# Optimization experiments

Hardware: AMD Instinct MI355X
Metric: run time of the kernel (lower is better)

## Reference

```python
import jax, jax.numpy as jnp
import numpy as np

N_NODES = 50000
N_EDGES = 1600000
N_FEAT, N_HID, N_CLASS = 256, 128, 64


def setup_inputs() -> dict:
    key = jax.random.key(0)
    ks = jax.random.split(key, 8)
    x = jax.random.normal(ks[0], (N_NODES, N_FEAT), dtype=jnp.float32)
    edge_index = jax.random.randint(ks[1], (2, N_EDGES), 0, N_NODES, dtype=jnp.int64)
    edge_weight = jax.random.uniform(ks[2], (N_EDGES,), dtype=jnp.float32)
    # Glorot-style init for GCNConv weights, zero bias (PyG defaults)
    W1 = jax.random.normal(ks[3], (N_FEAT, N_HID), dtype=jnp.float32) * (1.0 / np.sqrt(N_FEAT))
    b1 = jnp.zeros((N_HID,), dtype=jnp.float32)
    W2 = jax.random.normal(ks[4], (N_HID, N_CLASS), dtype=jnp.float32) * (1.0 / np.sqrt(N_HID))
    b2 = jnp.zeros((N_CLASS,), dtype=jnp.float32)
    return {"x": x, "edge_index": edge_index, "edge_weight": edge_weight,
            "W1": W1, "b1": b1, "W2": W2, "b2": b2}


def _gcn_norm(edge_index, edge_weight, num_nodes):
    # add self loops with weight 1 (GCNConv add_self_loops=True)
    loop = jnp.arange(num_nodes, dtype=edge_index.dtype)
    row = jnp.concatenate([edge_index[0], loop])
    col = jnp.concatenate([edge_index[1], loop])
    ew = jnp.concatenate([edge_weight, jnp.ones((num_nodes,), dtype=edge_weight.dtype)])
    # symmetric normalization: deg computed on target (col) nodes
    deg = jax.ops.segment_sum(ew, col, num_segments=num_nodes)
    dinv = jnp.where(deg > 0, jax.lax.rsqrt(deg), 0.0)
    norm = dinv[row] * ew * dinv[col]
    return row, col, norm


def _gcn_conv(h, row, col, norm, W, b, num_nodes):
    h = h @ W                       # [N, out]
    msgs = h[row] * norm[:, None]   # [E+N, out] gather + scale
    out = jax.ops.segment_sum(msgs, col, num_segments=num_nodes)  # scatter-add to targets
    return out + b


def reference(x, edge_index, edge_weight, W1, b1, W2, b2):
    n = x.shape[0]
    row, col, norm = _gcn_norm(edge_index, edge_weight, n)
    h = jax.nn.sigmoid(_gcn_conv(x, row, col, norm, W1, b1, n))
    out = jnp.tanh(_gcn_conv(h, row, col, norm, W2, b2, n))
    return out
```

## Files before the change

kernel.cpp:

```cpp
#include <hip/hip_runtime.h>
#include <math.h>

#define N_NODES 50000
#define N_EDGES 1600000
#define N_FEAT  256
#define N_HID   128
#define N_CLASS 64
#define SCAN_NBLK ((N_NODES + 1023) / 1024)
#define FIXSCALE 268435456.0f

__device__ __forceinline__ unsigned short f2bf(float f) {
  unsigned int u = __float_as_uint(f);
  unsigned int r = (u + 0x7fffu + ((u >> 16) & 1u)) >> 16;
  return (unsigned short)r;
}

__global__ __launch_bounds__(256) void deg_rank_kernel(
    const int* __restrict__ col, const float* __restrict__ ew,
    unsigned long long* __restrict__ packed, unsigned short* __restrict__ rank, int E) {
  int e = blockIdx.x * 256 + threadIdx.x;
  if (e >= E) return;
  int c = col[e];
  unsigned long long fix = (unsigned long long)__float2uint_rn(ew[e] * FIXSCALE);
  unsigned long long old = atomicAdd(&packed[c], (1ULL << 40) | fix);
  rank[e] = (unsigned short)(old >> 40);
}

__global__ __launch_bounds__(256) void scan1_kernel(
    const unsigned long long* __restrict__ packed, int* __restrict__ rowptr,
    int* __restrict__ partials, float* __restrict__ dinv) {
  __shared__ int wsum[4];
  __shared__ int woff[4];
  int t = threadIdx.x, b = blockIdx.x;
  int base = b * 1024 + t * 4;
  int v0 = 0, v1 = 0, v2 = 0, v3 = 0;
#pragma unroll
  for (int j = 0; j < 4; ++j) {
    int i = base + j;
    if (i < N_NODES) {
      unsigned long long p = packed[i];
      int c = (int)(p >> 40);
      float deg = (float)(long long)(p & 0xFFFFFFFFFFULL) * (1.0f / FIXSCALE);
      dinv[i] = rsqrtf(deg + 1.0f);
      if (j == 0) v0 = c; else if (j == 1) v1 = c; else if (j == 2) v2 = c; else v3 = c;
    }
  }
  int s1 = v0 + v1, s2 = s1 + v2, s3 = s2 + v3;
  int lane = t & 63, w = t >> 6;
  int inc = s3;
#pragma unroll
  for (int off = 1; off < 64; off <<= 1) {
    int u = __shfl_up(inc, off, 64);
    if (lane >= off) inc += u;
  }
  if (lane == 63) wsum[w] = inc;
  __syncthreads();
  if (t == 0) {
    int a = 0;
#pragma unroll
    for (int i = 0; i < 4; ++i) { woff[i] = a; a += wsum[i]; }
    partials[b] = a;
  }
  __syncthreads();
  int ex = woff[w] + inc - s3;
  if (base + 0 < N_NODES) rowptr[base + 0] = ex;
  if (base + 1 < N_NODES) rowptr[base + 1] = ex + v0;
  if (base + 2 < N_NODES) rowptr[base + 2] = ex + s1;
  if (base + 3 < N_NODES) rowptr[base + 3] = ex + s2;
}

__global__ void scan2_kernel(int* __restrict__ partials, int* __restrict__ rowptr) {
  if (threadIdx.x == 0 && blockIdx.x == 0) {
    int a = 0;
    for (int i = 0; i < SCAN_NBLK; ++i) { int x = partials[i]; partials[i] = a; a += x; }
    rowptr[N_NODES] = a;
  }
}

__global__ __launch_bounds__(256) void scan3_kernel(
    int* __restrict__ rowptr, const int* __restrict__ partials) {
  int i = blockIdx.x * 256 + threadIdx.x;
  if (i < N_NODES) rowptr[i] += partials[i >> 10];
}

__global__ __launch_bounds__(256) void scatter_kernel(
    const int* __restrict__ row, const int* __restrict__ col,
    const float* __restrict__ ew, const unsigned short* __restrict__ rank,
    const float* __restrict__ dinv, const int* __restrict__ rowptr,
    int2* __restrict__ ep, int E) {
  int e = blockIdx.x * 256 + threadIdx.x;
  if (e >= E) return;
  int r = row[e], c = col[e];
  float w = dinv[r] * ew[e] * dinv[c];
  int pos = rowptr[c] + (int)rank[e];
  ep[pos] = make_int2(r, __float_as_int(w));
}

template <int BN, int BK, int K>
__global__ __launch_bounds__(256) void gemm_kernel(
    const float* __restrict__ A, const float* __restrict__ B,
    unsigned short* __restrict__ C, int M) {
  constexpr int BM = 64;
  constexpr int TC = BN / 4;
  constexpr int TR = 256 / TC;
  constexpr int RM = BM / TR;
  __shared__ float As[BM][BK + 4];
  __shared__ float Bs[BK][BN];

  int t  = threadIdx.x;
  int m0 = blockIdx.x * BM;
  int tc = t % TC, tr = t / TC;

  float acc[RM][4];
#pragma unroll
  for (int r = 0; r < RM; ++r)
#pragma unroll
    for (int c = 0; c < 4; ++c) acc[r][c] = 0.f;

  for (int k0 = 0; k0 < K; k0 += BK) {
    constexpr int F4R = BK / 4;
#pragma unroll
    for (int p = 0; p < (BM * F4R) / 256; ++p) {
      int row = t / F4R + p * (256 / F4R);
      int c4  = t % F4R;
      int gr  = m0 + row;
      float4 v = make_float4(0.f, 0.f, 0.f, 0.f);
      if (gr < M) v = *(const float4*)&A[(size_t)gr * K + k0 + c4 * 4];
      *(float4*)&As[row][c4 * 4] = v;
    }
    constexpr int BF4 = BK * BN / 4;
#pragma unroll
    for (int p = 0; p < BF4 / 256; ++p) {
      int idx = p * 256 + t;
      int row = idx / (BN / 4), c4 = idx % (BN / 4);
      *(float4*)&Bs[row][c4 * 4] = *(const float4*)&B[(size_t)(k0 + row) * BN + c4 * 4];
    }
    __syncthreads();

    for (int kk = 0; kk < BK; kk += 4) {
      float4 b0 = *(const float4*)&Bs[kk + 0][tc * 4];
      float4 b1 = *(const float4*)&Bs[kk + 1][tc * 4];
      float4 b2 = *(const float4*)&Bs[kk + 2][tc * 4];
      float4 b3 = *(const float4*)&Bs[kk + 3][tc * 4];
#pragma unroll
      for (int r = 0; r < RM; ++r) {
        float4 a = *(const float4*)&As[tr * RM + r][kk];
        acc[r][0] = fmaf(a.x, b0.x, fmaf(a.y, b1.x, fmaf(a.z, b2.x, fmaf(a.w, b3.x, acc[r][0]))));
        acc[r][1] = fmaf(a.x, b0.y, fmaf(a.y, b1.y, fmaf(a.z, b2.y, fmaf(a.w, b3.y, acc[r][1]))));
        acc[r][2] = fmaf(a.x, b0.z, fmaf(a.y, b1.z, fmaf(a.z, b2.z, fmaf(a.w, b3.z, acc[r][2]))));
        acc[r][3] = fmaf(a.x, b0.w, fmaf(a.y, b1.w, fmaf(a.z, b2.w, fmaf(a.w, b3.w, acc[r][3]))));
      }
    }
    __syncthreads();
  }
#pragma unroll
  for (int r = 0; r < RM; ++r) {
    int gr = m0 + tr * RM + r;
    if (gr < M) {
      uint2 o;
      o.x = (unsigned int)f2bf(acc[r][0]) | ((unsigned int)f2bf(acc[r][1]) << 16);
      o.y = (unsigned int)f2bf(acc[r][2]) | ((unsigned int)f2bf(acc[r][3]) << 16);
      *(uint2*)&C[(size_t)gr * BN + tc * 4] = o;
    }
  }
}

__global__ __launch_bounds__(256) void agg128_kernel(
    const unsigned short* __restrict__ h, const int* __restrict__ rowptr,
    const int2* __restrict__ ep, const float* __restrict__ dinv,
    const float* __restrict__ bias, float* __restrict__ out, int n) {
  int wid  = (int)((blockIdx.x * 256 + threadIdx.x) >> 6);
  int lane = threadIdx.x & 63;
  if (wid >= n) return;
  int s = rowptr[wid], e_end = rowptr[wid + 1];
  unsigned int f2 = 2u * lane;
  float a0 = 0.f, a1 = 0.f, b0 = 0.f, b1 = 0.f,
        c0 = 0.f, c1 = 0.f, d0 = 0.f, d1 = 0.f;
  int e = s;
  for (; e + 3 < e_end; e += 4) {
    int2 p0 = ep[e], p1 = ep[e + 1], p2 = ep[e + 2], p3 = ep[e + 3];
    unsigned int h0 = *(const unsigned int*)(h + ((size_t)p0.x << 7) + f2);
    unsigned int h1 = *(const unsigned int*)(h + ((size_t)p1.x << 7) + f2);
    unsigned int h2 = *(const unsigned int*)(h + ((size_t)p2.x << 7) + f2);
    unsigned int h3 = *(const unsigned int*)(h + ((size_t)p3.x << 7) + f2);
    float w0 = __int_as_float(p0.y), w1 = __int_as_float(p1.y);
    float w2 = __int_as_float(p2.y), w3 = __int_as_float(p3.y);
    a0 = fmaf(w0, __uint_as_float(h0 << 16), a0);
    a1 = fmaf(w0, __uint_as_float(h0 & 0xffff0000u), a1);
    b0 = fmaf(w1, __uint_as_float(h1 << 16), b0);
    b1 = fmaf(w1, __uint_as_float(h1 & 0xffff0000u), b1);
    c0 = fmaf(w2, __uint_as_float(h2 << 16), c0);
    c1 = fmaf(w2, __uint_as_float(h2 & 0xffff0000u), c1);
    d0 = fmaf(w3, __uint_as_float(h3 << 16), d0);
    d1 = fmaf(w3, __uint_as_float(h3 & 0xffff0000u), d1);
  }
  for (; e < e_end; ++e) {
    int2 p0 = ep[e];
    unsigned int h0 = *(const unsigned int*)(h + ((size_t)p0.x << 7) + f2);
    float w0 = __int_as_float(p0.y);
    a0 = fmaf(w0, __uint_as_float(h0 << 16), a0);
    a1 = fmaf(w0, __uint_as_float(h0 & 0xffff0000u), a1);
  }
  float di = dinv[wid], sw = di * di;
  unsigned int hs = *(const unsigned int*)(h + ((size_t)wid << 7) + f2);
  a0 = fmaf(sw, __uint_as_float(hs << 16), a0);
  a1 = fmaf(sw, __uint_as_float(hs & 0xffff0000u), a1);
  float v0 = (a0 + b0) + (c0 + d0) + bias[f2];
  float v1 = (a1 + b1) + (c1 + d1) + bias[f2 + 1];
  v0 = 1.f / (1.f + expf(-v0));
  v1 = 1.f / (1.f + expf(-v1));
  *(float2*)&out[((size_t)wid << 7) + f2] = make_float2(v0, v1);
}

__global__ __launch_bounds__(256) void agg64_kernel(
    const unsigned short* __restrict__ h, const int* __restrict__ rowptr,
    const int2* __restrict__ ep, const float* __restrict__ dinv,
    const float* __restrict__ bias, float* __restrict__ out, int n) {
  int wid  = (int)((blockIdx.x * 256 + threadIdx.x) >> 6);
  int lane = threadIdx.x & 63;
  if (wid >= n) return;
  int half = lane >> 5, ll = lane & 31;
  unsigned int f2 = 2u * ll;
  int s = rowptr[wid], e_end = rowptr[wid + 1];
  float a0 = 0.f, a1 = 0.f, b0 = 0.f, b1 = 0.f,
        c0 = 0.f, c1 = 0.f, d0 = 0.f, d1 = 0.f;
  int e = s + half;
  for (; e + 6 < e_end; e += 8) {
    int2 p0 = ep[e], p1 = ep[e + 2], p2 = ep[e + 4], p3 = ep[e + 6];
    unsigned int h0 = *(const unsigned int*)(h + ((size_t)p0.x << 6) + f2);
    unsigned int h1 = *(const unsigned int*)(h + ((size_t)p1.x << 6) + f2);
    unsigned int h2 = *(const unsigned int*)(h + ((size_t)p2.x << 6) + f2);
    unsigned int h3 = *(const unsigned int*)(h + ((size_t)p3.x << 6) + f2);
    float w0 = __int_as_float(p0.y), w1 = __int_as_float(p1.y);
    float w2 = __int_as_float(p2.y), w3 = __int_as_float(p3.y);
    a0 = fmaf(w0, __uint_as_float(h0 << 16), a0);
    a1 = fmaf(w0, __uint_as_float(h0 & 0xffff0000u), a1);
    b0 = fmaf(w1, __uint_as_float(h1 << 16), b0);
    b1 = fmaf(w1, __uint_as_float(h1 & 0xffff0000u), b1);
    c0 = fmaf(w2, __uint_as_float(h2 << 16), c0);
    c1 = fmaf(w2, __uint_as_float(h2 & 0xffff0000u), c1);
    d0 = fmaf(w3, __uint_as_float(h3 << 16), d0);
    d1 = fmaf(w3, __uint_as_float(h3 & 0xffff0000u), d1);
  }
  for (; e < e_end; e += 2) {
    int2 p0 = ep[e];
    unsigned int h0 = *(const unsigned int*)(h + ((size_t)p0.x << 6) + f2);
    float w0 = __int_as_float(p0.y);
    a0 = fmaf(w0, __uint_as_float(h0 << 16), a0);
    a1 = fmaf(w0, __uint_as_float(h0 & 0xffff0000u), a1);
  }
  a0 = (a0 + b0) + (c0 + d0);
  a1 = (a1 + b1) + (c1 + d1);
  if (half == 0) {
    float di = dinv[wid], sw = di * di;
    unsigned int hs = *(const unsigned int*)(h + ((size_t)wid << 6) + f2);
    a0 = fmaf(sw, __uint_as_float(hs << 16), a0);
    a1 = fmaf(sw, __uint_as_float(hs & 0xffff0000u), a1);
  }
  a0 += __shfl_xor(a0, 32, 64);
  a1 += __shfl_xor(a1, 32, 64);
  if (half == 0) {
    float v0 = tanhf(a0 + bias[f2]);
    float v1 = tanhf(a1 + bias[f2 + 1]);
    *(float2*)&out[(size_t)wid * 64 + f2] = make_float2(v0, v1);
  }
}

extern "C" void kernel_launch(void* const* d_in, const int* in_sizes, int n_in,
                              void* d_out, int out_size, void* d_ws, size_t ws_size,
                              hipStream_t stream) {
  const float* x  = (const float*)d_in[0];
  const int*   ei = (const int*)d_in[1];
  const float* ew = (const float*)d_in[2];
  const float* W1 = (const float*)d_in[3];
  const float* b1 = (const float*)d_in[4];
  const float* W2 = (const float*)d_in[5];
  const float* b2 = (const float*)d_in[6];
  float* out = (float*)d_out;

  const int* row = ei;
  const int* col = ei + N_EDGES;

  char* ws = (char*)d_ws;
  size_t off = 0;
  auto alloc = [&](size_t bytes) {
    void* p = ws + off;
    off = (off + bytes + 255) & ~(size_t)255;
    return p;
  };
  unsigned long long* packed = (unsigned long long*)alloc(N_NODES * 8);
  int*   rowptr   = (int*)alloc((N_NODES + 1) * 4);
  float* dinv     = (float*)alloc(N_NODES * 4);
  int*   partials = (int*)alloc(SCAN_NBLK * 4);
  unsigned short* rank = (unsigned short*)alloc((size_t)N_EDGES * 2);
  int2*  ep       = (int2*)alloc((size_t)N_EDGES * 8);
  unsigned short* bufA = (unsigned short*)alloc((size_t)N_NODES * N_HID * 2);
  float*          bufB = (float*)alloc((size_t)N_NODES * N_HID * 4);
  unsigned short* bufC = (unsigned short*)alloc((size_t)N_NODES * N_CLASS * 2);

  hipMemsetAsync(packed, 0, N_NODES * 8, stream);

  int eblocks = (N_EDGES + 255) / 256;
  int nblocks = (N_NODES + 255) / 256;
  int gblocks = (N_NODES + 63) / 64;

  deg_rank_kernel<<<eblocks, 256, 0, stream>>>(col, ew, packed, rank, N_EDGES);
  scan1_kernel<<<SCAN_NBLK, 256, 0, stream>>>(packed, rowptr, partials, dinv);
  scan2_kernel<<<1, 64, 0, stream>>>(partials, rowptr);
  scan3_kernel<<<nblocks, 256, 0, stream>>>(rowptr, partials);
  scatter_kernel<<<eblocks, 256, 0, stream>>>(row, col, ew, rank, dinv, rowptr, ep, N_EDGES);

  gemm_kernel<N_HID, 64, N_FEAT><<<gblocks, 256, 0, stream>>>(x, W1, bufA, N_NODES);
  agg128_kernel<<<(N_NODES * 64 + 255) / 256, 256, 0, stream>>>(
      bufA, rowptr, ep, dinv, b1, bufB, N_NODES);

  gemm_kernel<N_CLASS, 64, N_HID><<<gblocks, 256, 0, stream>>>(bufB, W2, bufC, N_NODES);
  agg64_kernel<<<(N_NODES * 64 + 255) / 256, 256, 0, stream>>>(
      bufC, rowptr, ep, dinv, b2, out, N_NODES);
}
```

Measured before the change: 398.3 us.

## Use bf16 MFMA GEMMs with transposed bf16 weights and bf16 hidden activations

Replaces the fp32 FMA tiled GEMMs with a bf16 MFMA (16x16x32) kernel. The A and B tiles sit in swizzled LDS, and the weights are pre-transposed and converted to bf16 by a new small kernel. The first aggregation now writes its sigmoid output as bf16 instead of fp32, which halves the intermediate buffer traffic and lets the second GEMM read bf16 directly. The cost is lower precision on the inputs and the hidden layer, plus two extra tiny launches. Output stores are now scalar 16-bit writes.

Result: faster. 350.0 us (-12.1%).

```diff
diff --git a/kernel.cpp b/kernel.cpp
--- a/kernel.cpp
+++ b/kernel.cpp
@@ -9,10 +9,21 @@
 #define SCAN_NBLK ((N_NODES + 1023) / 1024)
 #define FIXSCALE 268435456.0f
 
-__device__ __forceinline__ unsigned short f2bf(float f) {
+typedef __attribute__((ext_vector_type(8))) short short8v;
+typedef __attribute__((ext_vector_type(4))) float float4v;
+
+__device__ __forceinline__ unsigned int f2bf(float f) {
   unsigned int u = __float_as_uint(f);
   unsigned int r = (u + 0x7fffu + ((u >> 16) & 1u)) >> 16;
-  return (unsigned short)r;
+  return r & 0xffffu;
+}
+
+__global__ __launch_bounds__(256) void transpose_w_kernel(
+    const float* __restrict__ W, unsigned short* __restrict__ WT, int K, int N) {
+  int i = blockIdx.x * 256 + threadIdx.x;
+  if (i >= N * K) return;
+  int n = i / K, k = i % K;
+  WT[i] = (unsigned short)f2bf(W[(size_t)k * N + n]);
 }
 
 __global__ __launch_bounds__(256) void deg_rank_kernel(
@@ -96,71 +107,91 @@
   ep[pos] = make_int2(r, __float_as_int(w));
 }
 
-template <int BN, int BK, int K>
-__global__ __launch_bounds__(256) void gemm_kernel(
-    const float* __restrict__ A, const float* __restrict__ B,
+template <int BN, int K, bool AFP32>
+__global__ __launch_bounds__(256) void mfma_gemm_kernel(
+    const void* __restrict__ Ain, const unsigned short* __restrict__ BT,
     unsigned short* __restrict__ C, int M) {
-  constexpr int BM = 64;
-  constexpr int TC = BN / 4;
-  constexpr int TR = 256 / TC;
-  constexpr int RM = BM / TR;
-  __shared__ float As[BM][BK + 4];
-  __shared__ float Bs[BK][BN];
-
-  int t  = threadIdx.x;
+  constexpr int BM = 64, BK = 64;
+  constexpr int NT = BN / 16;
+  __shared__ unsigned char AsB[BM * 128];
+  __shared__ unsigned char BsB[BN * 128];
+  int t = threadIdx.x;
+  int lane = t & 63, wv = t >> 6;
   int m0 = blockIdx.x * BM;
-  int tc = t % TC, tr = t / TC;
-
-  float acc[RM][4];
-#pragma unroll
-  for (int r = 0; r < RM; ++r)
-#pragma unroll
-    for (int c = 0; c < 4; ++c) acc[r][c] = 0.f;
+
+  float4v acc[NT];
+#pragma unroll
+  for (int i = 0; i < NT; ++i) acc[i] = (float4v){0.f, 0.f, 0.f, 0.f};
 
   for (int k0 = 0; k0 < K; k0 += BK) {
-    constexpr int F4R = BK / 4;
-#pragma unroll
-    for (int p = 0; p < (BM * F4R) / 256; ++p) {
-      int row = t / F4R + p * (256 / F4R);
-      int c4  = t % F4R;
-      int gr  = m0 + row;
-      float4 v = make_float4(0.f, 0.f, 0.f, 0.f);
-      if (gr < M) v = *(const float4*)&A[(size_t)gr * K + k0 + c4 * 4];
-      *(float4*)&As[row][c4 * 4] = v;
-    }
-    constexpr int BF4 = BK * BN / 4;
-#pragma unroll
-    for (int p = 0; p < BF4 / 256; ++p) {
-      int idx = p * 256 + t;
-      int row = idx / (BN / 4), c4 = idx % (BN / 4);
-      *(float4*)&Bs[row][c4 * 4] = *(const float4*)&B[(size_t)(k0 + row) * BN + c4 * 4];
+    {
+      int r = t >> 2, q = t & 3;
+      int gr = m0 + r;
+      unsigned int swz = (unsigned int)((r & 7) << 4);
+      uint4 o0 = make_uint4(0, 0, 0, 0), o1 = make_uint4(0, 0, 0, 0);
+      if constexpr (AFP32) {
+        const float* A = (const float*)Ain;
+        if (gr < M) {
+          const float* p = &A[(size_t)gr * K + k0 + q * 16];
+          float4 v0 = *(const float4*)(p + 0), v1 = *(const float4*)(p + 4);
+          float4 v2 = *(const float4*)(p + 8), v3 = *(const float4*)(p + 12);
+          o0.x = f2bf(v0.x) | (f2bf(v0.y) << 16); o0.y = f2bf(v0.z) | (f2bf(v0.w) << 16);
+          o0.z = f2bf(v1.x) | (f2bf(v1.y) << 16); o0.w = f2bf(v1.z) | (f2bf(v1.w) << 16);
+          o1.x = f2bf(v2.x) | (f2bf(v2.y) << 16); o1.y = f2bf(v2.z) | (f2bf(v2.w) << 16);
+          o1.z = f2bf(v3.x) | (f2bf(v3.y) << 16); o1.w = f2bf(v3.z) | (f2bf(v3.w) << 16);
+        }
+      } else {
+        const unsigned short* A = (const unsigned short*)Ain;
+        if (gr < M) {
+          const unsigned short* p = &A[(size_t)gr * K + k0 + q * 16];
+          o0 = *(const uint4*)(p);
+          o1 = *(const uint4*)(p + 8);
+        }
+      }
+      *(uint4*)(AsB + r * 128 + (((unsigned)(q * 32)) ^ swz)) = o0;
+      *(uint4*)(AsB + r * 128 + (((unsigned)(q * 32 + 16)) ^ swz)) = o1;
+    }
+    {
+      constexpr int BPT = BN / 2;
+      constexpr int TPR = 128 / BPT;
+      int br = t / TPR;
+      int bo = (t % TPR) * BPT;
+      unsigned int swz = (unsigned int)((br & 7) << 4);
+#pragma unroll
+      for (int s = 0; s < BPT / 16; ++s) {
+        uint4 v = *(const uint4*)&BT[(size_t)br * K + k0 + (bo + s * 16) / 2];
+        *(uint4*)(BsB + br * 128 + (((unsigned)(bo + s * 16)) ^ swz)) = v;
+      }
     }
     __syncthreads();
-
-    for (int kk = 0; kk < BK; kk += 4) {
-      float4 b0 = *(const float4*)&Bs[kk + 0][tc * 4];
-      float4 b1 = *(const float4*)&Bs[kk + 1][tc * 4];
-      float4 b2 = *(const float4*)&Bs[kk + 2][tc * 4];
-      float4 b3 = *(const float4*)&Bs[kk + 3][tc * 4];
-#pragma unroll
-      for (int r = 0; r < RM; ++r) {
-        float4 a = *(const float4*)&As[tr * RM + r][kk];
-        acc[r][0] = fmaf(a.x, b0.x, fmaf(a.y, b1.x, fmaf(a.z, b2.x, fmaf(a.w, b3.x, acc[r][0]))));
-        acc[r][1] = fmaf(a.x, b0.y, fmaf(a.y, b1.y, fmaf(a.z, b2.y, fmaf(a.w, b3.y, acc[r][1]))));
-        acc[r][2] = fmaf(a.x, b0.z, fmaf(a.y, b1.z, fmaf(a.z, b2.z, fmaf(a.w, b3.z, acc[r][2]))));
-        acc[r][3] = fmaf(a.x, b0.w, fmaf(a.y, b1.w, fmaf(a.z, b2.w, fmaf(a.w, b3.w, acc[r][3]))));
+    {
+      int ar = wv * 16 + (lane & 15);
+      int g = lane >> 4;
+      unsigned int aswz = (unsigned int)((ar & 7) << 4);
+      unsigned int bswz = (unsigned int)((lane & 7) << 4);
+#pragma unroll
+      for (int kk = 0; kk < BK; kk += 32) {
+        short8v af = *(const short8v*)(AsB + ar * 128 +
+                                       (((unsigned)(kk * 2 + g * 16)) ^ aswz));
+#pragma unroll
+        for (int nt = 0; nt < NT; ++nt) {
+          int brr = nt * 16 + (lane & 15);
+          short8v bf = *(const short8v*)(BsB + brr * 128 +
+                                         (((unsigned)(kk * 2 + g * 16)) ^ bswz));
+          acc[nt] = __builtin_amdgcn_mfma_f32_16x16x32_bf16(af, bf, acc[nt], 0, 0, 0);
+        }
       }
     }
     __syncthreads();
   }
-#pragma unroll
-  for (int r = 0; r < RM; ++r) {
-    int gr = m0 + tr * RM + r;
-    if (gr < M) {
-      uint2 o;
-      o.x = (unsigned int)f2bf(acc[r][0]) | ((unsigned int)f2bf(acc[r][1]) << 16);
-      o.y = (unsigned int)f2bf(acc[r][2]) | ((unsigned int)f2bf(acc[r][3]) << 16);
-      *(uint2*)&C[(size_t)gr * BN + tc * 4] = o;
+  int r0 = m0 + wv * 16 + (lane >> 4) * 4;
+  int c0 = lane & 15;
+#pragma unroll
+  for (int nt = 0; nt < NT; ++nt) {
+#pragma unroll
+    for (int j = 0; j < 4; ++j) {
+      int gr = r0 + j;
+      if (gr < M) C[(size_t)gr * BN + nt * 16 + c0] = (unsigned short)f2bf(acc[nt][j]);
     }
   }
 }
@@ -168,7 +199,7 @@
 __global__ __launch_bounds__(256) void agg128_kernel(
     const unsigned short* __restrict__ h, const int* __restrict__ rowptr,
     const int2* __restrict__ ep, const float* __restrict__ dinv,
-    const float* __restrict__ bias, float* __restrict__ out, int n) {
+    const float* __restrict__ bias, unsigned short* __restrict__ out, int n) {
   int wid  = (int)((blockIdx.x * 256 + threadIdx.x) >> 6);
   int lane = threadIdx.x & 63;
   if (wid >= n) return;
@@ -209,7 +240,8 @@
   float v1 = (a1 + b1) + (c1 + d1) + bias[f2 + 1];
   v0 = 1.f / (1.f + expf(-v0));
   v1 = 1.f / (1.f + expf(-v1));
-  *(float2*)&out[((size_t)wid << 7) + f2] = make_float2(v0, v1);
+  unsigned int o = f2bf(v0) | (f2bf(v1) << 16);
+  *(unsigned int*)(out + ((size_t)wid << 7) + f2) = o;
 }
 
 __global__ __launch_bounds__(256) void agg64_kernel(
@@ -294,8 +326,10 @@
   int*   partials = (int*)alloc(SCAN_NBLK * 4);
   unsigned short* rank = (unsigned short*)alloc((size_t)N_EDGES * 2);
   int2*  ep       = (int2*)alloc((size_t)N_EDGES * 8);
+  unsigned short* W1T  = (unsigned short*)alloc((size_t)N_HID * N_FEAT * 2);
+  unsigned short* W2T  = (unsigned short*)alloc((size_t)N_CLASS * N_HID * 2);
   unsigned short* bufA = (unsigned short*)alloc((size_t)N_NODES * N_HID * 2);
-  float*          bufB = (float*)alloc((size_t)N_NODES * N_HID * 4);
+  unsigned short* bufB = (unsigned short*)alloc((size_t)N_NODES * N_HID * 2);
   unsigned short* bufC = (unsigned short*)alloc((size_t)N_NODES * N_CLASS * 2);
 
   hipMemsetAsync(packed, 0, N_NODES * 8, stream);
@@ -303,6 +337,9 @@
   int eblocks = (N_EDGES + 255) / 256;
   int nblocks = (N_NODES + 255) / 256;
   int gblocks = (N_NODES + 63) / 64;
+
+  transpose_w_kernel<<<(N_HID * N_FEAT + 255) / 256, 256, 0, stream>>>(W1, W1T, N_FEAT, N_HID);
+  transpose_w_kernel<<<(N_CLASS * N_HID + 255) / 256, 256, 0, stream>>>(W2, W2T, N_HID, N_CLASS);
 
   deg_rank_kernel<<<eblocks, 256, 0, stream>>>(col, ew, packed, rank, N_EDGES);
   scan1_kernel<<<SCAN_NBLK, 256, 0, stream>>>(packed, rowptr, partials, dinv);
@@ -310,11 +347,11 @@
   scan3_kernel<<<nblocks, 256, 0, stream>>>(rowptr, partials);
   scatter_kernel<<<eblocks, 256, 0, stream>>>(row, col, ew, rank, dinv, rowptr, ep, N_EDGES);
 
-  gemm_kernel<N_HID, 64, N_FEAT><<<gblocks, 256, 0, stream>>>(x, W1, bufA, N_NODES);
+  mfma_gemm_kernel<N_HID, N_FEAT, true><<<gblocks, 256, 0, stream>>>(x, W1T, bufA, N_NODES);
   agg128_kernel<<<(N_NODES * 64 + 255) / 256, 256, 0, stream>>>(
       bufA, rowptr, ep, dinv, b1, bufB, N_NODES);
 
-  gemm_kernel<N_CLASS, 64, N_HID><<<gblocks, 256, 0, stream>>>(bufB, W2, bufC, N_NODES);
+  mfma_gemm_kernel<N_CLASS, N_HID, false><<<gblocks, 256, 0, stream>>>(bufB, W2T, bufC, N_NODES);
   agg64_kernel<<<(N_NODES * 64 + 255) / 256, 256, 0, stream>>>(
       bufC, rowptr, ep, dinv, b2, out, N_NODES);
 }
```
